# Performance work log

Hardware: AMD Instinct MI355X
Metric: run time of the kernel (lower is better)

## Reference

```python
import jax, jax.numpy as jnp
import numpy as np

B, C, H, W = 8, 512, 64, 64
M = C // 8  # query/key channels
EPS = 1e-6

def setup_inputs() -> dict:
    key = jax.random.key(0)
    ks = jax.random.split(key, 8)
    s_in = 0.02
    return {
        "x": jax.random.normal(ks[0], (B, C, H, W), dtype=jnp.float32),
        "Wq": jax.random.normal(ks[1], (M, C), dtype=jnp.float32) * s_in,
        "bq": jnp.zeros((M,), dtype=jnp.float32),
        "Wk": jax.random.normal(ks[2], (M, C), dtype=jnp.float32) * s_in,
        "bk": jnp.zeros((M,), dtype=jnp.float32),
        "Wv": jax.random.normal(ks[3], (C, C), dtype=jnp.float32) * s_in,
        "bv": jnp.zeros((C,), dtype=jnp.float32),
        "gamma": jax.random.uniform(ks[4], (1,), dtype=jnp.float32) * 0.5,
    }

def _l2_norm(t):
    # normalize over channel dim (axis=-2), per position; matches torch.norm(p=2, dim=-2)
    return t / jnp.linalg.norm(t, axis=-2, keepdims=True)

def reference(x, Wq, bq, Wk, bk, Wv, bv, gamma):
    b, c, h, w = x.shape
    n = h * w
    xf = x.reshape(b, c, n)                               # [b,c,n]
    # 1x1 convs as channel GEMMs
    Q = jnp.einsum('mc,bcn->bmn', Wq, xf) + bq[None, :, None]   # [b,m,n]
    K = jnp.einsum('mc,bcn->bmn', Wk, xf) + bk[None, :, None]   # [b,m,n]
    V = jnp.einsum('dc,bcn->bdn', Wv, xf) + bv[None, :, None]   # [b,c,n]
    Qn = _l2_norm(Q).transpose(0, 2, 1)                   # [b,n,m]
    Kn = _l2_norm(K)                                      # [b,m,n]
    # denominator: 1 / (N + Q . sum_n(K))
    tailor = 1.0 / (n + jnp.einsum('bnm,bm->bn', Qn, Kn.sum(axis=-1) + EPS))  # [b,n]
    value_sum = V.sum(axis=-1)                            # [b,c]
    matrix = jnp.einsum('bmn,bcn->bmc', Kn, V)            # [b,m,c] (O(N) contraction)
    matrix_sum = value_sum[:, :, None] + jnp.einsum('bnm,bmc->bcn', Qn, matrix)  # [b,c,n]
    weight_value = matrix_sum * tailor[:, None, :]        # [b,c,n]
    return x + gamma * weight_value.reshape(b, c, h, w)
```

## Files before the change

kernel.cpp:

```cpp
#include <hip/hip_runtime.h>
#include <hip/hip_bf16.h>

constexpr int B = 8;
constexpr int C = 512;
constexpr int M = 64;
constexpr int N = 4096;
constexpr float EPS = 1e-6f;
constexpr int NTS = 16;
constexpr int LDP = 72;
constexpr int LDPF = 68;

typedef __attribute__((ext_vector_type(8))) short short8v;
typedef __attribute__((ext_vector_type(4))) short short4v;
typedef __attribute__((ext_vector_type(4))) float f32x4;

__device__ __forceinline__ short f2b(float f) {
  union { __hip_bfloat16 h; short s; } u;
  u.h = __float2bfloat16(f);
  return u.s;
}
__device__ __forceinline__ float b2f(short s) {
  union { __hip_bfloat16 h; short s2; } u;
  u.s2 = s;
  return __bfloat162float(u.h);
}

__global__ __launch_bounds__(256) void prep_kernel(
    const float* __restrict__ Wq, const float* __restrict__ Wk,
    const float* __restrict__ Wv, short* __restrict__ Wq_bf,
    short* __restrict__ Wk_bf, short* __restrict__ Wv_bf,
    float* __restrict__ Ksum, float* __restrict__ xsum) {
  const int id = blockIdx.x * 256 + threadIdx.x;
  const int stride = gridDim.x * 256;
  for (int i = id; i < C * M / 4; i += stride) {
    const float4 a = reinterpret_cast<const float4*>(Wq)[i];
    const float4 b = reinterpret_cast<const float4*>(Wk)[i];
    short4v sa = {f2b(a.x), f2b(a.y), f2b(a.z), f2b(a.w)};
    short4v sb = {f2b(b.x), f2b(b.y), f2b(b.z), f2b(b.w)};
    reinterpret_cast<short4v*>(Wq_bf)[i] = sa;
    reinterpret_cast<short4v*>(Wk_bf)[i] = sb;
  }
  for (int i = id; i < C * C / 4; i += stride) {
    const float4 a = reinterpret_cast<const float4*>(Wv)[i];
    short4v sa = {f2b(a.x), f2b(a.y), f2b(a.z), f2b(a.w)};
    reinterpret_cast<short4v*>(Wv_bf)[i] = sa;
  }
  for (int i = id; i < B * M + B * C; i += stride) {
    if (i < B * M) Ksum[i] = 0.f;
    else xsum[i - B * M] = 0.f;
  }
}

__global__ __launch_bounds__(256) void prepx_kernel(
    const float* __restrict__ x, short* __restrict__ x_bf,
    short* __restrict__ xT_bf, float* __restrict__ xsum) {
  __shared__ short lt[64 * LDP];
  __shared__ float red[256];
  const int t = threadIdx.x;
  const int nb = blockIdx.x * 64;
  const int cb = blockIdx.y * 64;
  const int b = blockIdx.z;
  const int r = t >> 2, q = t & 3;
  const float* xp = x + ((size_t)b * C + cb + r) * N + nb + q * 16;
  float4 v[4];
#pragma unroll
  for (int i = 0; i < 4; ++i) v[i] = *reinterpret_cast<const float4*>(xp + 4 * i);
  short tmp[16];
  float s = 0.f;
#pragma unroll
  for (int i = 0; i < 4; ++i) {
    tmp[4 * i + 0] = f2b(v[i].x); tmp[4 * i + 1] = f2b(v[i].y);
    tmp[4 * i + 2] = f2b(v[i].z); tmp[4 * i + 3] = f2b(v[i].w);
    s += v[i].x + v[i].y + v[i].z + v[i].w;
  }
  {
    short* dst = x_bf + ((size_t)b * C + cb + r) * N + nb + q * 16;
    *reinterpret_cast<short8v*>(dst) = *reinterpret_cast<const short8v*>(&tmp[0]);
    *reinterpret_cast<short8v*>(dst + 8) = *reinterpret_cast<const short8v*>(&tmp[8]);
  }
#pragma unroll
  for (int i = 0; i < 16; ++i) lt[(q * 16 + i) * LDP + r] = tmp[i];
  red[t] = s;
  __syncthreads();
  if (t < 64) {
    const float rs = red[4 * t] + red[4 * t + 1] + red[4 * t + 2] + red[4 * t + 3];
    atomicAdd(&xsum[b * C + cb + t], rs);
  }
  {
    const int n = t >> 2;
    short* dst = xT_bf + ((size_t)b * N + nb + n) * C + cb + q * 16;
    *reinterpret_cast<short8v*>(dst) = *reinterpret_cast<const short8v*>(&lt[n * LDP + q * 16]);
    *reinterpret_cast<short8v*>(dst + 8) = *reinterpret_cast<const short8v*>(&lt[n * LDP + q * 16 + 8]);
  }
}

__global__ __launch_bounds__(256) void qk_kernel(
    const short* __restrict__ xT_bf, const short* __restrict__ Wq_bf,
    const float* __restrict__ bq, const short* __restrict__ Wk_bf,
    const float* __restrict__ bk, short* __restrict__ QnT,
    short* __restrict__ KnB, float* __restrict__ Ksum) {
  __shared__ short aq[64 * LDP];
  __shared__ short ak[64 * LDP];
  __shared__ short bx[64 * LDP];
  __shared__ float colred[2][4][64];
  __shared__ float rsq[2][64];
  const int t = threadIdx.x;
  const int n0 = blockIdx.x * 64;
  const int b = blockIdx.y;
  const int w = t >> 6, l = t & 63, l15 = l & 15, kg = l >> 4;
  const int sr = t >> 2, sko = (t & 3) * 16;
  f32x4 accQ[4], accK[4];
#pragma unroll
  for (int i = 0; i < 4; ++i) { accQ[i] = f32x4{0.f, 0.f, 0.f, 0.f}; accK[i] = f32x4{0.f, 0.f, 0.f, 0.f}; }

  for (int c0 = 0; c0 < C; c0 += 64) {
    __syncthreads();
    *reinterpret_cast<short8v*>(&aq[sr * LDP + sko]) =
        *reinterpret_cast<const short8v*>(&Wq_bf[sr * C + c0 + sko]);
    *reinterpret_cast<short8v*>(&aq[sr * LDP + sko + 8]) =
        *reinterpret_cast<const short8v*>(&Wq_bf[sr * C + c0 + sko + 8]);
    *reinterpret_cast<short8v*>(&ak[sr * LDP + sko]) =
        *reinterpret_cast<const short8v*>(&Wk_bf[sr * C + c0 + sko]);
    *reinterpret_cast<short8v*>(&ak[sr * LDP + sko + 8]) =
        *reinterpret_cast<const short8v*>(&Wk_bf[sr * C + c0 + sko + 8]);
    const short* xg = &xT_bf[((size_t)b * N + n0 + sr) * C + c0 + sko];
    *reinterpret_cast<short8v*>(&bx[sr * LDP + sko]) = *reinterpret_cast<const short8v*>(xg);
    *reinterpret_cast<short8v*>(&bx[sr * LDP + sko + 8]) = *reinterpret_cast<const short8v*>(xg + 8);
    __syncthreads();
#pragma unroll
    for (int ks = 0; ks < 2; ++ks) {
      const short8v afq = *reinterpret_cast<const short8v*>(&aq[(w * 16 + l15) * LDP + ks * 32 + kg * 8]);
      const short8v afk = *reinterpret_cast<const short8v*>(&ak[(w * 16 + l15) * LDP + ks * 32 + kg * 8]);
#pragma unroll
      for (int tc = 0; tc < 4; ++tc) {
        const short8v bf = *reinterpret_cast<const short8v*>(&bx[(tc * 16 + l15) * LDP + ks * 32 + kg * 8]);
        accQ[tc] = __builtin_amdgcn_mfma_f32_16x16x32_bf16(afq, bf, accQ[tc], 0, 0, 0);
        accK[tc] = __builtin_amdgcn_mfma_f32_16x16x32_bf16(afk, bf, accK[tc], 0, 0, 0);
      }
    }
  }
  {
    const float4 q4 = *reinterpret_cast<const float4*>(&bq[w * 16 + kg * 4]);
    const float4 k4 = *reinterpret_cast<const float4*>(&bk[w * 16 + kg * 4]);
    const float bqa[4] = {q4.x, q4.y, q4.z, q4.w};
    const float bka[4] = {k4.x, k4.y, k4.z, k4.w};
#pragma unroll
    for (int tc = 0; tc < 4; ++tc)
#pragma unroll
      for (int r = 0; r < 4; ++r) { accQ[tc][r] += bqa[r]; accK[tc][r] += bka[r]; }
  }
#pragma unroll
  for (int tc = 0; tc < 4; ++tc) {
    float vq = accQ[tc][0] * accQ[tc][0] + accQ[tc][1] * accQ[tc][1] +
               accQ[tc][2] * accQ[tc][2] + accQ[tc][3] * accQ[tc][3];
    float vk = accK[tc][0] * accK[tc][0] + accK[tc][1] * accK[tc][1] +
               accK[tc][2] * accK[tc][2] + accK[tc][3] * accK[tc][3];
    vq += __shfl_xor(vq, 16, 64); vq += __shfl_xor(vq, 32, 64);
    vk += __shfl_xor(vk, 16, 64); vk += __shfl_xor(vk, 32, 64);
    if (l < 16) { colred[0][w][tc * 16 + l] = vq; colred[1][w][tc * 16 + l] = vk; }
  }
  __syncthreads();
  if (t < 128) {
    const int which = t >> 6, n = t & 63;
    const float s = colred[which][0][n] + colred[which][1][n] +
                    colred[which][2][n] + colred[which][3][n];
    rsq[which][n] = 1.0f / sqrtf(s);
  }
  __syncthreads();
  float ksr[4] = {0.f, 0.f, 0.f, 0.f};
#pragma unroll
  for (int tc = 0; tc < 4; ++tc) {
    const float rq = rsq[0][tc * 16 + l15], rk = rsq[1][tc * 16 + l15];
#pragma unroll
    for (int r = 0; r < 4; ++r) { accQ[tc][r] *= rq; accK[tc][r] *= rk; ksr[r] += accK[tc][r]; }
  }
#pragma unroll
  for (int r = 0; r < 4; ++r) {
    float s = ksr[r];
    s += __shfl_xor(s, 1, 64); s += __shfl_xor(s, 2, 64);
    s += __shfl_xor(s, 4, 64); s += __shfl_xor(s, 8, 64);
    if (l15 == 0) atomicAdd(&Ksum[b * M + w * 16 + kg * 4 + r], s);
  }
#pragma unroll
  for (int tc = 0; tc < 4; ++tc) {
    short4v q4 = {f2b(accQ[tc][0]), f2b(accQ[tc][1]), f2b(accQ[tc][2]), f2b(accQ[tc][3])};
    *reinterpret_cast<short4v*>(&aq[(tc * 16 + l15) * LDP + w * 16 + kg * 4]) = q4;
#pragma unroll
    for (int r = 0; r < 4; ++r)
      ak[(w * 16 + kg * 4 + r) * LDP + tc * 16 + l15] = f2b(accK[tc][r]);
  }
  __syncthreads();
  {
    short* qg = QnT + ((size_t)b * N + n0 + sr) * M + sko;
    *reinterpret_cast<short8v*>(qg) = *reinterpret_cast<const short8v*>(&aq[sr * LDP + sko]);
    *reinterpret_cast<short8v*>(qg + 8) = *reinterpret_cast<const short8v*>(&aq[sr * LDP + sko + 8]);
    short* kg2 = KnB + ((size_t)b * M + sr) * N + n0 + sko;
    *reinterpret_cast<short8v*>(kg2) = *reinterpret_cast<const short8v*>(&ak[sr * LDP + sko]);
    *reinterpret_cast<short8v*>(kg2 + 8) = *reinterpret_cast<const short8v*>(&ak[sr * LDP + sko + 8]);
  }
}

__global__ __launch_bounds__(256) void s_kernel(
    const short* __restrict__ x_bf, const short* __restrict__ KnB,
    short* __restrict__ Spart) {
  __shared__ short sm[2 * 64 * LDP];
  short* ka = sm;
  short* xb = sm + 64 * LDP;
  const int t = threadIdx.x;
  const int c0 = blockIdx.x * 64;
  const int nt = blockIdx.y;
  const int b = blockIdx.z;
  const int w = t >> 6, l = t & 63, l15 = l & 15, kg = l >> 4;
  const int sr = t >> 2, sko = (t & 3) * 16;
  f32x4 acc[4];
#pragma unroll
  for (int i = 0; i < 4; ++i) acc[i] = f32x4{0.f, 0.f, 0.f, 0.f};
  constexpr int ITERS = N / NTS / 64;
  const int nbase = nt * (N / NTS);
  for (int it = 0; it < ITERS; ++it) {
    const int nk = nbase + it * 64;
    __syncthreads();
    {
      const short* kp = &KnB[((size_t)b * M + sr) * N + nk + sko];
      *reinterpret_cast<short8v*>(&ka[sr * LDP + sko]) = *reinterpret_cast<const short8v*>(kp);
      *reinterpret_cast<short8v*>(&ka[sr * LDP + sko + 8]) = *reinterpret_cast<const short8v*>(kp + 8);
      const short* xp = &x_bf[((size_t)b * C + c0 + sr) * N + nk + sko];
      *reinterpret_cast<short8v*>(&xb[sr * LDP + sko]) = *reinterpret_cast<const short8v*>(xp);
      *reinterpret_cast<short8v*>(&xb[sr * LDP + sko + 8]) = *reinterpret_cast<const short8v*>(xp + 8);
    }
    __syncthreads();
#pragma unroll
    for (int ks = 0; ks < 2; ++ks) {
      const short8v af = *reinterpret_cast<const short8v*>(&ka[(w * 16 + l15) * LDP + ks * 32 + kg * 8]);
#pragma unroll
      for (int tc = 0; tc < 4; ++tc) {
        const short8v bf = *reinterpret_cast<const short8v*>(&xb[(tc * 16 + l15) * LDP + ks * 32 + kg * 8]);
        acc[tc] = __builtin_amdgcn_mfma_f32_16x16x32_bf16(af, bf, acc[tc], 0, 0, 0);
      }
    }
  }
  __syncthreads();
#pragma unroll
  for (int tc = 0; tc < 4; ++tc)
#pragma unroll
    for (int r = 0; r < 4; ++r)
      sm[(w * 16 + kg * 4 + r) * LDP + tc * 16 + l15] = f2b(acc[tc][r]);
  __syncthreads();
  {
    short* gp = Spart + (((size_t)nt * B + b) * M + sr) * C + c0 + sko;
    *reinterpret_cast<short8v*>(gp) = *reinterpret_cast<const short8v*>(&sm[sr * LDP + sko]);
    *reinterpret_cast<short8v*>(gp + 8) = *reinterpret_cast<const short8v*>(&sm[sr * LDP + sko + 8]);
  }
}

__global__ __launch_bounds__(256) void matm_kernel(
    const short* __restrict__ Wv_bf, const float* __restrict__ bv,
    const short* __restrict__ Spart, const float* __restrict__ xsum,
    const float* __restrict__ Ksum, short* __restrict__ matMT,
    float* __restrict__ vsum) {
  __shared__ short wa[64 * LDP];
  __shared__ short sb[64 * LDP];
  __shared__ float xs[64];
  const int t = threadIdx.x;
  const int c0 = blockIdx.x * 64;
  const int b = blockIdx.y;
  const int w = t >> 6, l = t & 63, l15 = l & 15, kg = l >> 4;
  const int sr = t >> 2, sko = (t & 3) * 16;
  f32x4 acc[4];
#pragma unroll
  for (int i = 0; i < 4; ++i) acc[i] = f32x4{0.f, 0.f, 0.f, 0.f};
  float vacc = 0.f;
  for (int k0 = 0; k0 < C; k0 += 64) {
    __syncthreads();
    *reinterpret_cast<short8v*>(&wa[sr * LDP + sko]) =
        *reinterpret_cast<const short8v*>(&Wv_bf[(size_t)(c0 + sr) * C + k0 + sko]);
    *reinterpret_cast<short8v*>(&wa[sr * LDP + sko + 8]) =
        *reinterpret_cast<const short8v*>(&Wv_bf[(size_t)(c0 + sr) * C + k0 + sko + 8]);
    {
      float sacc[16];
#pragma unroll
      for (int j = 0; j < 16; ++j) sacc[j] = 0.f;
#pragma unroll 4
      for (int nt2 = 0; nt2 < NTS; ++nt2) {
        const short* sp = Spart + (((size_t)nt2 * B + b) * M + sr) * C + k0 + sko;
        const short8v p0 = *reinterpret_cast<const short8v*>(sp);
        const short8v p1 = *reinterpret_cast<const short8v*>(sp + 8);
#pragma unroll
        for (int j = 0; j < 8; ++j) { sacc[j] += b2f(p0[j]); sacc[8 + j] += b2f(p1[j]); }
      }
      short tmp[16];
#pragma unroll
      for (int j = 0; j < 16; ++j) tmp[j] = f2b(sacc[j]);
      *reinterpret_cast<short8v*>(&sb[sr * LDP + sko]) = *reinterpret_cast<const short8v*>(&tmp[0]);
      *reinterpret_cast<short8v*>(&sb[sr * LDP + sko + 8]) = *reinterpret_cast<const short8v*>(&tmp[8]);
    }
    if (t < 64) xs[t] = xsum[b * C + k0 + t];
    __syncthreads();
#pragma unroll
    for (int ks = 0; ks < 2; ++ks) {
      const short8v af = *reinterpret_cast<const short8v*>(&wa[(w * 16 + l15) * LDP + ks * 32 + kg * 8]);
#pragma unroll
      for (int tc = 0; tc < 4; ++tc) {
        const short8v bf = *reinterpret_cast<const short8v*>(&sb[(tc * 16 + l15) * LDP + ks * 32 + kg * 8]);
        acc[tc] = __builtin_amdgcn_mfma_f32_16x16x32_bf16(af, bf, acc[tc], 0, 0, 0);
      }
    }
    if (t < 64) {
      float v = 0.f;
#pragma unroll 8
      for (int kk = 0; kk < 64; ++kk) v = fmaf(b2f(wa[t * LDP + kk]), xs[kk], v);
      vacc += v;
    }
  }
  __syncthreads();
  {
    const float4 b4 = *reinterpret_cast<const float4*>(&bv[c0 + w * 16 + kg * 4]);
    const float bva[4] = {b4.x, b4.y, b4.z, b4.w};
#pragma unroll
    for (int tc = 0; tc < 4; ++tc) {
      const float ksm = Ksum[b * M + tc * 16 + l15];
#pragma unroll
      for (int r = 0; r < 4; ++r)
        wa[(w * 16 + kg * 4 + r) * LDP + tc * 16 + l15] = f2b(acc[tc][r] + bva[r] * ksm);
    }
  }
  __syncthreads();
  {
    short* gp = matMT + ((size_t)b * C + c0 + sr) * M + sko;
    *reinterpret_cast<short8v*>(gp) = *reinterpret_cast<const short8v*>(&wa[sr * LDP + sko]);
    *reinterpret_cast<short8v*>(gp + 8) = *reinterpret_cast<const short8v*>(&wa[sr * LDP + sko + 8]);
  }
  if (t < 64) vsum[b * C + c0 + t] = vacc + 4096.0f * bv[c0 + t];
}

__global__ __launch_bounds__(256) void final_kernel(
    const short* __restrict__ x_bf, const short* __restrict__ QnT,
    const float* __restrict__ Ksum, const short* __restrict__ matMT,
    const float* __restrict__ vsum, const float* __restrict__ gamma,
    float* __restrict__ out) {
  __shared__ short qb[64 * LDP];
  __shared__ short ab[64 * LDP];
  __shared__ float bo[64 * LDPF];
  __shared__ float ke[64];
  __shared__ float tl[64];
  __shared__ float red2[256];
  const int t = threadIdx.x;
  const int n0 = blockIdx.x * 64;
  const int cy = blockIdx.y;
  const int b = blockIdx.z;
  const int w = t >> 6, l = t & 63, l15 = l & 15, kg = l >> 4;
  const int sr = t >> 2, sko = (t & 3) * 16;
  {
    const short* qg = &QnT[((size_t)b * N + n0 + sr) * M + sko];
    *reinterpret_cast<short8v*>(&qb[sr * LDP + sko]) = *reinterpret_cast<const short8v*>(qg);
    *reinterpret_cast<short8v*>(&qb[sr * LDP + sko + 8]) = *reinterpret_cast<const short8v*>(qg + 8);
  }
  if (t < 64) ke[t] = Ksum[b * M + t] + EPS;
  __syncthreads();
  {
    const int n = t & 63, mq = t >> 6;
    float d = 0.f;
#pragma unroll
    for (int j = 0; j < 16; ++j) d = fmaf(b2f(qb[n * LDP + mq * 16 + j]), ke[mq * 16 + j], d);
    red2[t] = d;
  }
  __syncthreads();
  if (t < 64)
    tl[t] = 1.0f / (4096.0f + red2[t] + red2[64 + t] + red2[128 + t] + red2[192 + t]);
  const float g = gamma[0];
  for (int cc = 0; cc < 4; ++cc) {
    const int c0 = cy * 256 + cc * 64;
    __syncthreads();
    {
      const short* mp = &matMT[((size_t)b * C + c0 + sr) * M + sko];
      *reinterpret_cast<short8v*>(&ab[sr * LDP + sko]) = *reinterpret_cast<const short8v*>(mp);
      *reinterpret_cast<short8v*>(&ab[sr * LDP + sko + 8]) = *reinterpret_cast<const short8v*>(mp + 8);
    }
    __syncthreads();
    short8v xr0, xr1;
    {
      const short* xp = &x_bf[((size_t)b * C + c0 + sr) * N + n0 + sko];
      xr0 = *reinterpret_cast<const short8v*>(xp);
      xr1 = *reinterpret_cast<const short8v*>(xp + 8);
    }
    f32x4 acc[4];
#pragma unroll
    for (int i = 0; i < 4; ++i) acc[i] = f32x4{0.f, 0.f, 0.f, 0.f};
#pragma unroll
    for (int ks = 0; ks < 2; ++ks) {
      const short8v af = *reinterpret_cast<const short8v*>(&ab[(w * 16 + l15) * LDP + ks * 32 + kg * 8]);
#pragma unroll
      for (int tc = 0; tc < 4; ++tc) {
        const short8v bf = *reinterpret_cast<const short8v*>(&qb[(tc * 16 + l15) * LDP + ks * 32 + kg * 8]);
        acc[tc] = __builtin_amdgcn_mfma_f32_16x16x32_bf16(af, bf, acc[tc], 0, 0, 0);
      }
    }
#pragma unroll
    for (int tc = 0; tc < 4; ++tc)
#pragma unroll
      for (int r = 0; r < 4; ++r)
        bo[(w * 16 + kg * 4 + r) * LDPF + tc * 16 + l15] = acc[tc][r];
    __syncthreads();
    {
      const int c = c0 + sr;
      const float vs = vsum[b * C + c];
      const size_t off = ((size_t)b * C + c) * N + n0 + sko;
#pragma unroll
      for (int i = 0; i < 4; ++i) {
        const float4 dv = *reinterpret_cast<const float4*>(&bo[sr * LDPF + sko + 4 * i]);
        const float4 tv = *reinterpret_cast<const float4*>(&tl[sko + 4 * i]);
        float4 o;
        o.x = b2f(i * 4 + 0 < 8 ? xr0[i * 4 + 0] : xr1[i * 4 - 8]) + g * tv.x * (vs + dv.x);
        o.y = b2f(i * 4 + 1 < 8 ? xr0[(i * 4 + 1) & 7] : xr1[(i * 4 + 1) & 7]) + g * tv.y * (vs + dv.y);
        o.z = b2f(i * 4 + 2 < 8 ? xr0[(i * 4 + 2) & 7] : xr1[(i * 4 + 2) & 7]) + g * tv.z * (vs + dv.z);
        o.w = b2f(i * 4 + 3 < 8 ? xr0[(i * 4 + 3) & 7] : xr1[(i * 4 + 3) & 7]) + g * tv.w * (vs + dv.w);
        *reinterpret_cast<float4*>(&out[off + 4 * i]) = o;
      }
    }
  }
}

extern "C" void kernel_launch(void* const* d_in, const int* in_sizes, int n_in,
                              void* d_out, int out_size, void* d_ws, size_t ws_size,
                              hipStream_t stream) {
  (void)in_sizes; (void)n_in; (void)out_size; (void)ws_size;
  const float* x = (const float*)d_in[0];
  const float* Wq = (const float*)d_in[1];
  const float* bq = (const float*)d_in[2];
  const float* Wk = (const float*)d_in[3];
  const float* bk = (const float*)d_in[4];
  const float* Wv = (const float*)d_in[5];
  const float* bv = (const float*)d_in[6];
  const float* gamma = (const float*)d_in[7];
  float* out = (float*)d_out;

  char* wp = (char*)d_ws;
  short* Wq_bf = (short*)wp;  wp += (size_t)C * M * 2;
  short* Wk_bf = (short*)wp;  wp += (size_t)C * M * 2;
  short* Wv_bf = (short*)wp;  wp += (size_t)C * C * 2;
  short* x_bf  = (short*)wp;  wp += (size_t)B * C * N * 2;
  short* xT_bf = (short*)wp;  wp += (size_t)B * N * C * 2;
  short* KnB   = (short*)wp;  wp += (size_t)B * M * N * 2;
  short* QnT   = (short*)wp;  wp += (size_t)B * N * M * 2;
  short* matMT = (short*)wp;  wp += (size_t)B * C * M * 2;
  short* Spart = (short*)wp;  wp += (size_t)NTS * B * M * C * 2;
  float* Ksum  = (float*)wp;  wp += (size_t)B * M * 4;
  float* xsum  = (float*)wp;  wp += (size_t)B * C * 4;
  float* vsum  = (float*)wp;  wp += (size_t)B * C * 4;

  prep_kernel<<<256, 256, 0, stream>>>(Wq, Wk, Wv, Wq_bf, Wk_bf, Wv_bf, Ksum, xsum);
  prepx_kernel<<<dim3(N / 64, C / 64, B), 256, 0, stream>>>(x, x_bf, xT_bf, xsum);
  qk_kernel<<<dim3(N / 64, B), 256, 0, stream>>>(xT_bf, Wq_bf, bq, Wk_bf, bk, QnT, KnB, Ksum);
  s_kernel<<<dim3(C / 64, NTS, B), 256, 0, stream>>>(x_bf, KnB, Spart);
  matm_kernel<<<dim3(C / 64, B), 256, 0, stream>>>(Wv_bf, bv, Spart, xsum, Ksum, matMT, vsum);
  final_kernel<<<dim3(N / 64, 2, B), 256, 0, stream>>>(x_bf, QnT, Ksum, matMT, vsum, gamma, out);
}
```

Measured before the change: 220.2 us.

## Fuse x conversion, QK projection and K·x^T partials into one pass over x

Removes the prepx and s kernels. qks_kernel now reads fp32 x directly, converts it to bf16 in registers, computes Q/K, and reuses the kept x tiles to produce per-64-column partial K·x^T products and xsum. A new sreduce kernel sums the 64 partials before matm, and final_kernel reads fp32 x instead of the bf16 copy. This drops the bf16 x and xT intermediates and the extra reads of x. In exchange it adds a large partial buffer, higher register pressure from holding all x tiles per block, and a final pass with fewer blocks.

```diff
diff --git a/kernel.cpp b/kernel.cpp
--- a/kernel.cpp
+++ b/kernel.cpp
@@ -6,7 +6,7 @@
 constexpr int M = 64;
 constexpr int N = 4096;
 constexpr float EPS = 1e-6f;
-constexpr int NTS = 16;
+constexpr int NPART = N / 64;
 constexpr int LDP = 72;
 constexpr int LDPF = 68;
 
@@ -51,69 +51,33 @@
   }
 }
 
-__global__ __launch_bounds__(256) void prepx_kernel(
-    const float* __restrict__ x, short* __restrict__ x_bf,
-    short* __restrict__ xT_bf, float* __restrict__ xsum) {
-  __shared__ short lt[64 * LDP];
-  __shared__ float red[256];
-  const int t = threadIdx.x;
-  const int nb = blockIdx.x * 64;
-  const int cb = blockIdx.y * 64;
-  const int b = blockIdx.z;
-  const int r = t >> 2, q = t & 3;
-  const float* xp = x + ((size_t)b * C + cb + r) * N + nb + q * 16;
-  float4 v[4];
-#pragma unroll
-  for (int i = 0; i < 4; ++i) v[i] = *reinterpret_cast<const float4*>(xp + 4 * i);
-  short tmp[16];
-  float s = 0.f;
-#pragma unroll
-  for (int i = 0; i < 4; ++i) {
-    tmp[4 * i + 0] = f2b(v[i].x); tmp[4 * i + 1] = f2b(v[i].y);
-    tmp[4 * i + 2] = f2b(v[i].z); tmp[4 * i + 3] = f2b(v[i].w);
-    s += v[i].x + v[i].y + v[i].z + v[i].w;
-  }
-  {
-    short* dst = x_bf + ((size_t)b * C + cb + r) * N + nb + q * 16;
-    *reinterpret_cast<short8v*>(dst) = *reinterpret_cast<const short8v*>(&tmp[0]);
-    *reinterpret_cast<short8v*>(dst + 8) = *reinterpret_cast<const short8v*>(&tmp[8]);
-  }
-#pragma unroll
-  for (int i = 0; i < 16; ++i) lt[(q * 16 + i) * LDP + r] = tmp[i];
-  red[t] = s;
-  __syncthreads();
-  if (t < 64) {
-    const float rs = red[4 * t] + red[4 * t + 1] + red[4 * t + 2] + red[4 * t + 3];
-    atomicAdd(&xsum[b * C + cb + t], rs);
-  }
-  {
-    const int n = t >> 2;
-    short* dst = xT_bf + ((size_t)b * N + nb + n) * C + cb + q * 16;
-    *reinterpret_cast<short8v*>(dst) = *reinterpret_cast<const short8v*>(&lt[n * LDP + q * 16]);
-    *reinterpret_cast<short8v*>(dst + 8) = *reinterpret_cast<const short8v*>(&lt[n * LDP + q * 16 + 8]);
-  }
-}
-
-__global__ __launch_bounds__(256) void qk_kernel(
-    const short* __restrict__ xT_bf, const short* __restrict__ Wq_bf,
+__global__ __launch_bounds__(256, 2) void qks_kernel(
+    const float* __restrict__ x, const short* __restrict__ Wq_bf,
     const float* __restrict__ bq, const short* __restrict__ Wk_bf,
     const float* __restrict__ bk, short* __restrict__ QnT,
-    short* __restrict__ KnB, float* __restrict__ Ksum) {
+    float* __restrict__ Ksum, short* __restrict__ Spart,
+    float* __restrict__ xsum) {
   __shared__ short aq[64 * LDP];
   __shared__ short ak[64 * LDP];
   __shared__ short bx[64 * LDP];
   __shared__ float colred[2][4][64];
   __shared__ float rsq[2][64];
+  __shared__ float red[256];
   const int t = threadIdx.x;
-  const int n0 = blockIdx.x * 64;
+  const int nt = blockIdx.x;
+  const int n0 = nt * 64;
   const int b = blockIdx.y;
   const int w = t >> 6, l = t & 63, l15 = l & 15, kg = l >> 4;
   const int sr = t >> 2, sko = (t & 3) * 16;
+  const int cr = t & 63, ng = t >> 6;
   f32x4 accQ[4], accK[4];
 #pragma unroll
   for (int i = 0; i < 4; ++i) { accQ[i] = f32x4{0.f, 0.f, 0.f, 0.f}; accK[i] = f32x4{0.f, 0.f, 0.f, 0.f}; }
-
-  for (int c0 = 0; c0 < C; c0 += 64) {
+  short8v xkeep[8][2];
+
+#pragma unroll
+  for (int p = 0; p < 8; ++p) {
+    const int c0 = p * 64;
     __syncthreads();
     *reinterpret_cast<short8v*>(&aq[sr * LDP + sko]) =
         *reinterpret_cast<const short8v*>(&Wq_bf[sr * C + c0 + sko]);
@@ -123,9 +87,22 @@
         *reinterpret_cast<const short8v*>(&Wk_bf[sr * C + c0 + sko]);
     *reinterpret_cast<short8v*>(&ak[sr * LDP + sko + 8]) =
         *reinterpret_cast<const short8v*>(&Wk_bf[sr * C + c0 + sko + 8]);
-    const short* xg = &xT_bf[((size_t)b * N + n0 + sr) * C + c0 + sko];
-    *reinterpret_cast<short8v*>(&bx[sr * LDP + sko]) = *reinterpret_cast<const short8v*>(xg);
-    *reinterpret_cast<short8v*>(&bx[sr * LDP + sko + 8]) = *reinterpret_cast<const short8v*>(xg + 8);
+    {
+      const float* xg = x + ((size_t)b * C + c0 + cr) * N + n0 + ng * 16;
+      float4 v[4];
+#pragma unroll
+      for (int i = 0; i < 4; ++i) v[i] = *reinterpret_cast<const float4*>(xg + 4 * i);
+      short tmp[16];
+#pragma unroll
+      for (int i = 0; i < 4; ++i) {
+        tmp[4 * i + 0] = f2b(v[i].x); tmp[4 * i + 1] = f2b(v[i].y);
+        tmp[4 * i + 2] = f2b(v[i].z); tmp[4 * i + 3] = f2b(v[i].w);
+      }
+      xkeep[p][0] = *reinterpret_cast<const short8v*>(&tmp[0]);
+      xkeep[p][1] = *reinterpret_cast<const short8v*>(&tmp[8]);
+#pragma unroll
+      for (int i = 0; i < 16; ++i) bx[(ng * 16 + i) * LDP + cr] = tmp[i];
+    }
     __syncthreads();
 #pragma unroll
     for (int ks = 0; ks < 2; ++ks) {
@@ -194,68 +171,70 @@
     short* qg = QnT + ((size_t)b * N + n0 + sr) * M + sko;
     *reinterpret_cast<short8v*>(qg) = *reinterpret_cast<const short8v*>(&aq[sr * LDP + sko]);
     *reinterpret_cast<short8v*>(qg + 8) = *reinterpret_cast<const short8v*>(&aq[sr * LDP + sko + 8]);
-    short* kg2 = KnB + ((size_t)b * M + sr) * N + n0 + sko;
-    *reinterpret_cast<short8v*>(kg2) = *reinterpret_cast<const short8v*>(&ak[sr * LDP + sko]);
-    *reinterpret_cast<short8v*>(kg2 + 8) = *reinterpret_cast<const short8v*>(&ak[sr * LDP + sko + 8]);
-  }
-}
-
-__global__ __launch_bounds__(256) void s_kernel(
-    const short* __restrict__ x_bf, const short* __restrict__ KnB,
-    short* __restrict__ Spart) {
-  __shared__ short sm[2 * 64 * LDP];
-  short* ka = sm;
-  short* xb = sm + 64 * LDP;
-  const int t = threadIdx.x;
-  const int c0 = blockIdx.x * 64;
-  const int nt = blockIdx.y;
-  const int b = blockIdx.z;
-  const int w = t >> 6, l = t & 63, l15 = l & 15, kg = l >> 4;
-  const int sr = t >> 2, sko = (t & 3) * 16;
-  f32x4 acc[4];
-#pragma unroll
-  for (int i = 0; i < 4; ++i) acc[i] = f32x4{0.f, 0.f, 0.f, 0.f};
-  constexpr int ITERS = N / NTS / 64;
-  const int nbase = nt * (N / NTS);
-  for (int it = 0; it < ITERS; ++it) {
-    const int nk = nbase + it * 64;
-    __syncthreads();
+  }
+
+#pragma unroll
+  for (int p = 0; p < 8; ++p) {
+    const int c0 = p * 64;
+    __syncthreads();
+    *reinterpret_cast<short8v*>(&bx[cr * LDP + ng * 16]) = xkeep[p][0];
+    *reinterpret_cast<short8v*>(&bx[cr * LDP + ng * 16 + 8]) = xkeep[p][1];
+    __syncthreads();
+    f32x4 sacc[4];
+#pragma unroll
+    for (int i = 0; i < 4; ++i) sacc[i] = f32x4{0.f, 0.f, 0.f, 0.f};
+#pragma unroll
+    for (int ks = 0; ks < 2; ++ks) {
+      const short8v af = *reinterpret_cast<const short8v*>(&ak[(w * 16 + l15) * LDP + ks * 32 + kg * 8]);
+#pragma unroll
+      for (int tc = 0; tc < 4; ++tc) {
+        const short8v bf = *reinterpret_cast<const short8v*>(&bx[(tc * 16 + l15) * LDP + ks * 32 + kg * 8]);
+        sacc[tc] = __builtin_amdgcn_mfma_f32_16x16x32_bf16(af, bf, sacc[tc], 0, 0, 0);
+      }
+    }
     {
-      const short* kp = &KnB[((size_t)b * M + sr) * N + nk + sko];
-      *reinterpret_cast<short8v*>(&ka[sr * LDP + sko]) = *reinterpret_cast<const short8v*>(kp);
-      *reinterpret_cast<short8v*>(&ka[sr * LDP + sko + 8]) = *reinterpret_cast<const short8v*>(kp + 8);
-      const short* xp = &x_bf[((size_t)b * C + c0 + sr) * N + nk + sko];
-      *reinterpret_cast<short8v*>(&xb[sr * LDP + sko]) = *reinterpret_cast<const short8v*>(xp);
-      *reinterpret_cast<short8v*>(&xb[sr * LDP + sko + 8]) = *reinterpret_cast<const short8v*>(xp + 8);
-    }
-    __syncthreads();
-#pragma unroll
-    for (int ks = 0; ks < 2; ++ks) {
-      const short8v af = *reinterpret_cast<const short8v*>(&ka[(w * 16 + l15) * LDP + ks * 32 + kg * 8]);
-#pragma unroll
-      for (int tc = 0; tc < 4; ++tc) {
-        const short8v bf = *reinterpret_cast<const short8v*>(&xb[(tc * 16 + l15) * LDP + ks * 32 + kg * 8]);
-        acc[tc] = __builtin_amdgcn_mfma_f32_16x16x32_bf16(af, bf, acc[tc], 0, 0, 0);
-      }
-    }
-  }
-  __syncthreads();
-#pragma unroll
-  for (int tc = 0; tc < 4; ++tc)
-#pragma unroll
-    for (int r = 0; r < 4; ++r)
-      sm[(w * 16 + kg * 4 + r) * LDP + tc * 16 + l15] = f2b(acc[tc][r]);
-  __syncthreads();
-  {
-    short* gp = Spart + (((size_t)nt * B + b) * M + sr) * C + c0 + sko;
-    *reinterpret_cast<short8v*>(gp) = *reinterpret_cast<const short8v*>(&sm[sr * LDP + sko]);
-    *reinterpret_cast<short8v*>(gp + 8) = *reinterpret_cast<const short8v*>(&sm[sr * LDP + sko + 8]);
-  }
+      float s = 0.f;
+#pragma unroll
+      for (int j = 0; j < 8; ++j) s += b2f(xkeep[p][0][j]) + b2f(xkeep[p][1][j]);
+      red[t] = s;
+    }
+    __syncthreads();
+    if (t < 64)
+      atomicAdd(&xsum[b * C + c0 + t], red[t] + red[64 + t] + red[128 + t] + red[192 + t]);
+#pragma unroll
+    for (int tc = 0; tc < 4; ++tc)
+#pragma unroll
+      for (int r = 0; r < 4; ++r)
+        aq[(w * 16 + kg * 4 + r) * LDP + tc * 16 + l15] = f2b(sacc[tc][r]);
+    __syncthreads();
+    {
+      short* gp = Spart + (((size_t)nt * B + b) * M + sr) * C + c0 + sko;
+      *reinterpret_cast<short8v*>(gp) = *reinterpret_cast<const short8v*>(&aq[sr * LDP + sko]);
+      *reinterpret_cast<short8v*>(gp + 8) = *reinterpret_cast<const short8v*>(&aq[sr * LDP + sko + 8]);
+    }
+  }
+}
+
+__global__ __launch_bounds__(256) void sreduce_kernel(const short* __restrict__ Spart,
+                                                      short* __restrict__ S_bf) {
+  const int i2 = blockIdx.x * 256 + threadIdx.x;
+  const size_t stride = (size_t)B * M * C;
+  const short* p = Spart + (size_t)i2 * 2;
+  float s0 = 0.f, s1 = 0.f;
+#pragma unroll 8
+  for (int nt = 0; nt < NPART; ++nt) {
+    const short* q = p + nt * stride;
+    s0 += b2f(q[0]);
+    s1 += b2f(q[1]);
+  }
+  short* o = S_bf + (size_t)i2 * 2;
+  o[0] = f2b(s0);
+  o[1] = f2b(s1);
 }
 
 __global__ __launch_bounds__(256) void matm_kernel(
     const short* __restrict__ Wv_bf, const float* __restrict__ bv,
-    const short* __restrict__ Spart, const float* __restrict__ xsum,
+    const short* __restrict__ S_bf, const float* __restrict__ xsum,
     const float* __restrict__ Ksum, short* __restrict__ matMT,
     float* __restrict__ vsum) {
   __shared__ short wa[64 * LDP];
@@ -276,24 +255,10 @@
         *reinterpret_cast<const short8v*>(&Wv_bf[(size_t)(c0 + sr) * C + k0 + sko]);
     *reinterpret_cast<short8v*>(&wa[sr * LDP + sko + 8]) =
         *reinterpret_cast<const short8v*>(&Wv_bf[(size_t)(c0 + sr) * C + k0 + sko + 8]);
-    {
-      float sacc[16];
-#pragma unroll
-      for (int j = 0; j < 16; ++j) sacc[j] = 0.f;
-#pragma unroll 4
-      for (int nt2 = 0; nt2 < NTS; ++nt2) {
-        const short* sp = Spart + (((size_t)nt2 * B + b) * M + sr) * C + k0 + sko;
-        const short8v p0 = *reinterpret_cast<const short8v*>(sp);
-        const short8v p1 = *reinterpret_cast<const short8v*>(sp + 8);
-#pragma unroll
-        for (int j = 0; j < 8; ++j) { sacc[j] += b2f(p0[j]); sacc[8 + j] += b2f(p1[j]); }
-      }
-      short tmp[16];
-#pragma unroll
-      for (int j = 0; j < 16; ++j) tmp[j] = f2b(sacc[j]);
-      *reinterpret_cast<short8v*>(&sb[sr * LDP + sko]) = *reinterpret_cast<const short8v*>(&tmp[0]);
-      *reinterpret_cast<short8v*>(&sb[sr * LDP + sko + 8]) = *reinterpret_cast<const short8v*>(&tmp[8]);
-    }
+    *reinterpret_cast<short8v*>(&sb[sr * LDP + sko]) =
+        *reinterpret_cast<const short8v*>(&S_bf[((size_t)b * M + sr) * C + k0 + sko]);
+    *reinterpret_cast<short8v*>(&sb[sr * LDP + sko + 8]) =
+        *reinterpret_cast<const short8v*>(&S_bf[((size_t)b * M + sr) * C + k0 + sko + 8]);
     if (t < 64) xs[t] = xsum[b * C + k0 + t];
     __syncthreads();
 #pragma unroll
@@ -334,7 +299,7 @@
 }
 
 __global__ __launch_bounds__(256) void final_kernel(
-    const short* __restrict__ x_bf, const short* __restrict__ QnT,
+    const float* __restrict__ x, const short* __restrict__ QnT,
     const float* __restrict__ Ksum, const short* __restrict__ matMT,
     const float* __restrict__ vsum, const float* __restrict__ gamma,
     float* __restrict__ out) {
@@ -346,8 +311,7 @@
   __shared__ float red2[256];
   const int t = threadIdx.x;
   const int n0 = blockIdx.x * 64;
-  const int cy = blockIdx.y;
-  const int b = blockIdx.z;
+  const int b = blockIdx.y;
   const int w = t >> 6, l = t & 63, l15 = l & 15, kg = l >> 4;
   const int sr = t >> 2, sko = (t & 3) * 16;
   {
@@ -368,8 +332,7 @@
   if (t < 64)
     tl[t] = 1.0f / (4096.0f + red2[t] + red2[64 + t] + red2[128 + t] + red2[192 + t]);
   const float g = gamma[0];
-  for (int cc = 0; cc < 4; ++cc) {
-    const int c0 = cy * 256 + cc * 64;
+  for (int c0 = 0; c0 < C; c0 += 64) {
     __syncthreads();
     {
       const short* mp = &matMT[((size_t)b * C + c0 + sr) * M + sko];
@@ -377,12 +340,6 @@
       *reinterpret_cast<short8v*>(&ab[sr * LDP + sko + 8]) = *reinterpret_cast<const short8v*>(mp + 8);
     }
     __syncthreads();
-    short8v xr0, xr1;
-    {
-      const short* xp = &x_bf[((size_t)b * C + c0 + sr) * N + n0 + sko];
-      xr0 = *reinterpret_cast<const short8v*>(xp);
-      xr1 = *reinterpret_cast<const short8v*>(xp + 8);
-    }
     f32x4 acc[4];
 #pragma unroll
     for (int i = 0; i < 4; ++i) acc[i] = f32x4{0.f, 0.f, 0.f, 0.f};
@@ -407,13 +364,14 @@
       const size_t off = ((size_t)b * C + c) * N + n0 + sko;
 #pragma unroll
       for (int i = 0; i < 4; ++i) {
+        const float4 xv = *reinterpret_cast<const float4*>(&x[off + 4 * i]);
         const float4 dv = *reinterpret_cast<const float4*>(&bo[sr * LDPF + sko + 4 * i]);
         const float4 tv = *reinterpret_cast<const float4*>(&tl[sko + 4 * i]);
         float4 o;
-        o.x = b2f(i * 4 + 0 < 8 ? xr0[i * 4 + 0] : xr1[i * 4 - 8]) + g * tv.x * (vs + dv.x);
-        o.y = b2f(i * 4 + 1 < 8 ? xr0[(i * 4 + 1) & 7] : xr1[(i * 4 + 1) & 7]) + g * tv.y * (vs + dv.y);
-        o.z = b2f(i * 4 + 2 < 8 ? xr0[(i * 4 + 2) & 7] : xr1[(i * 4 + 2) & 7]) + g * tv.z * (vs + dv.z);
-        o.w = b2f(i * 4 + 3 < 8 ? xr0[(i * 4 + 3) & 7] : xr1[(i * 4 + 3) & 7]) + g * tv.w * (vs + dv.w);
+        o.x = xv.x + g * tv.x * (vs + dv.x);
+        o.y = xv.y + g * tv.y * (vs + dv.y);
+        o.z = xv.z + g * tv.z * (vs + dv.z);
+        o.w = xv.w + g * tv.w * (vs + dv.w);
         *reinterpret_cast<float4*>(&out[off + 4 * i]) = o;
       }
     }
@@ -438,20 +396,17 @@
   short* Wq_bf = (short*)wp;  wp += (size_t)C * M * 2;
   short* Wk_bf = (short*)wp;  wp += (size_t)C * M * 2;
   short* Wv_bf = (short*)wp;  wp += (size_t)C * C * 2;
-  short* x_bf  = (short*)wp;  wp += (size_t)B * C * N * 2;
-  short* xT_bf = (short*)wp;  wp += (size_t)B * N * C * 2;
-  short* KnB   = (short*)wp;  wp += (size_t)B * M * N * 2;
   short* QnT   = (short*)wp;  wp += (size_t)B * N * M * 2;
   short* matMT = (short*)wp;  wp += (size_t)B * C * M * 2;
-  short* Spart = (short*)wp;  wp += (size_t)NTS * B * M * C * 2;
+  short* S_bf  = (short*)wp;  wp += (size_t)B * M * C * 2;
+  short* Spart = (short*)wp;  wp += (size_t)NPART * B * M * C * 2;
   float* Ksum  = (float*)wp;  wp += (size_t)B * M * 4;
   float* xsum  = (float*)wp;  wp += (size_t)B * C * 4;
   float* vsum  = (float*)wp;  wp += (size_t)B * C * 4;
 
   prep_kernel<<<256, 256, 0, stream>>>(Wq, Wk, Wv, Wq_bf, Wk_bf, Wv_bf, Ksum, xsum);
-  prepx_kernel<<<dim3(N / 64, C / 64, B), 256, 0, stream>>>(x, x_bf, xT_bf, xsum);
-  qk_kernel<<<dim3(N / 64, B), 256, 0, stream>>>(xT_bf, Wq_bf, bq, Wk_bf, bk, QnT, KnB, Ksum);
-  s_kernel<<<dim3(C / 64, NTS, B), 256, 0, stream>>>(x_bf, KnB, Spart);
-  matm_kernel<<<dim3(C / 64, B), 256, 0, stream>>>(Wv_bf, bv, Spart, xsum, Ksum, matMT, vsum);
-  final_kernel<<<dim3(N / 64, 2, B), 256, 0, stream>>>(x_bf, QnT, Ksum, matMT, vsum, gamma, out);
-}
+  qks_kernel<<<dim3(N / 64, B), 256, 0, stream>>>(x, Wq_bf, bq, Wk_bf, bk, QnT, Ksum, Spart, xsum);
+  sreduce_kernel<<<B * M * C / 2 / 256, 256, 0, stream>>>(Spart, S_bf);
+  matm_kernel<<<dim3(C / 64, B), 256, 0, stream>>>(Wv_bf, bv, S_bf, xsum, Ksum, matMT, vsum);
+  final_kernel<<<dim3(N / 64, B), 256, 0, stream>>>(x, QnT, Ksum, matMT, vsum, gamma, out);
+}
```

Measured after the change: 185.8 us. 15.6% less time.
